# Kernel tuning notes

Hardware: AMD Instinct MI355X
Metric: run time of the kernel (lower is better)

Reference implementation:

```python
import jax, jax.numpy as jnp
import numpy as np
from jax import lax

B = 16384
N_NUM = 32
N_CAT = 16
D = 256
D_HID = 512
N_LAYERS = 8
VOCAB = 100001  # total_cats + 1
OUT_DIM = 2
TOT_FEAT = N_NUM + N_CAT
EPS = 1e-5


def _layernorm(x, g, b):
    mu = jnp.mean(x, axis=-1, keepdims=True)
    var = jnp.mean(jnp.square(x - mu), axis=-1, keepdims=True)
    return (x - mu) * lax.rsqrt(var + EPS) * g + b


def setup_inputs() -> dict:
    key = jax.random.key(0)
    ks = jax.random.split(key, 16)
    s = 0.02
    return {
        "x_numerical": jax.random.normal(ks[0], (B, N_NUM, 1), dtype=jnp.float32),
        "x_categorical_idx": jax.random.randint(ks[1], (B, N_CAT), 0, VOCAB - 1, dtype=jnp.int32),
        # per-feature Linear(1, D): weight [N_NUM, D], bias [N_NUM, D]
        "w_num": jax.random.normal(ks[2], (N_NUM, D), dtype=jnp.float32) * s,
        "b_num": jnp.zeros((N_NUM, D), dtype=jnp.float32),
        "cat_embed": jax.random.normal(ks[3], (VOCAB, D), dtype=jnp.float32) * s,
        "W_first": jax.random.normal(ks[4], (TOT_FEAT * D, D), dtype=jnp.float32) * s,
        "b_first": jnp.zeros((D,), dtype=jnp.float32),
        # stacked block params, leading dim = N_LAYERS
        "ln_g": jnp.ones((N_LAYERS, D), dtype=jnp.float32),
        "ln_b": jnp.zeros((N_LAYERS, D), dtype=jnp.float32),
        "W1s": jax.random.normal(ks[5], (N_LAYERS, D, D_HID), dtype=jnp.float32) * s,
        "b1s": jnp.zeros((N_LAYERS, D_HID), dtype=jnp.float32),
        "W2s": jax.random.normal(ks[6], (N_LAYERS, D_HID, D), dtype=jnp.float32) * s,
        "b2s": jnp.zeros((N_LAYERS, D), dtype=jnp.float32),
        "g_f": jnp.ones((D,), dtype=jnp.float32),
        "beta_f": jnp.zeros((D,), dtype=jnp.float32),
        "W_head": jax.random.normal(ks[7], (D, OUT_DIM), dtype=jnp.float32) * s,
        "b_head": jnp.zeros((OUT_DIM,), dtype=jnp.float32),
    }


def reference(x_numerical, x_categorical_idx, w_num, b_num, cat_embed,
              W_first, b_first, ln_g, ln_b, W1s, b1s, W2s, b2s,
              g_f, beta_f, W_head, b_head):
    # numerical embeddings: per-feature Linear(1, D), vectorized over features
    x_val = x_numerical[:, :, 0:1]                       # [B, N_NUM, 1]
    x_n_emb = x_val * w_num[None] + b_num[None]          # [B, N_NUM, D]
    x_c_emb = cat_embed[x_categorical_idx]               # [B, N_CAT, D]
    x = jnp.concatenate([x_n_emb, x_c_emb], axis=1)      # [B, TOT_FEAT, D]
    x = x.reshape(x.shape[0], -1)                        # [B, TOT_FEAT*D]
    x = x @ W_first + b_first                            # [B, D]

    def block(h, params):
        g, bn, W1, b1, W2, b2 = params
        out = _layernorm(h, g, bn)
        out = jax.nn.relu(out @ W1 + b1)                 # dropout = identity (eval)
        out = out @ W2 + b2
        return h + out, None

    x, _ = lax.scan(block, x, (ln_g, ln_b, W1s, b1s, W2s, b2s))
    x = _layernorm(x, g_f, beta_f)
    logits = x @ W_head + b_head                         # [B, OUT_DIM]
    return logits
```

## Files before the change

### kernel.cpp

```cpp
#include <hip/hip_runtime.h>

typedef unsigned short u16;
typedef unsigned int u32;
typedef __attribute__((ext_vector_type(8))) short bf16x8;
typedef __attribute__((ext_vector_type(4))) float f32x4;

#define LDK 72

__device__ __forceinline__ u16 f2bf(float f) {
    u32 u = __float_as_uint(f);
    u += 0x7fffu + ((u >> 16) & 1u);
    return (u16)(u >> 16);
}

__device__ __forceinline__ f32x4 mfma16(bf16x8 a, bf16x8 b, f32x4 c) {
    return __builtin_amdgcn_mfma_f32_16x16x32_bf16(a, b, c, 0, 0, 0);
}


__global__ __launch_bounds__(256) void prep_u_kernel(
    const float* __restrict__ w_num, const float* __restrict__ b_num,
    const float* __restrict__ W_first, float* __restrict__ U, float* __restrict__ P)
{
    __shared__ float wrow[256];
    __shared__ float brow[256];
    int j = threadIdx.x, f = blockIdx.x;
    wrow[j] = w_num[f * 256 + j];
    brow[j] = b_num[f * 256 + j];
    __syncthreads();
    float au = 0.f, ap = 0.f;
    for (int k = 0; k < 256; k++) {
        float w = W_first[(size_t)((f << 8) + k) * 256 + j];
        au = fmaf(wrow[k], w, au);
        ap = fmaf(brow[k], w, ap);
    }
    U[f * 256 + j] = au;
    P[f * 256 + j] = ap;
}

__global__ __launch_bounds__(256) void prep_c0_kernel(
    const float* __restrict__ b_first, const float* __restrict__ P, float* __restrict__ c0)
{
    int j = threadIdx.x;
    float a = b_first[j];
    for (int f = 0; f < 32; f++) a += P[f * 256 + j];
    c0[j] = a;
}

__global__ __launch_bounds__(256) void transpose_kernel(
    const float* __restrict__ in, u16* __restrict__ out,
    int R, int C, int ldo, int k_off, size_t in_stride, size_t out_stride)
{
    __shared__ float t[64][65];
    in  += (size_t)blockIdx.z * in_stride;
    out += (size_t)blockIdx.z * out_stride;
    const int tid = threadIdx.x;
    const int r0 = blockIdx.x * 64, c0 = blockIdx.y * 64;
#pragma unroll
    for (int i = 0; i < 16; i++) {
        int e = tid + i * 256;
        int r = e >> 6, c = e & 63;
        float v = (r0 + r < R) ? in[(size_t)(r0 + r) * C + c0 + c] : 0.f;
        t[c][r] = v;
    }
    __syncthreads();
#pragma unroll
    for (int i = 0; i < 2; i++) {
        int e = tid + i * 256;
        int c = e >> 3, r8 = (e & 7) * 8;
        u16 tmp[8];
#pragma unroll
        for (int x = 0; x < 8; x++) tmp[x] = f2bf(t[c][r8 + x]);
        *(bf16x8*)&out[(size_t)(c0 + c) * ldo + k_off + r0 + r8] = *(bf16x8*)tmp;
    }
}

#define FBM 32

#define GATHER(KQ, G0, G1)                                                    \
    {                                                                         \
        int chunk = tid;                                                      \
        int r = chunk >> 4, c4 = chunk & 15;                                  \
        int k = (KQ) + c4 * 4;                                                \
        if (k < 4096) {                                                       \
            int rowi = sidx[r * 16 + (k >> 8)];                               \
            G0 = *(const float4*)&cemb[(size_t)rowi * 256 + (k & 255)];       \
        } else if (k < 4128) {                                                \
            int c = k - 4096;                                                 \
            G0.x = sx[r * 32 + c];     G0.y = sx[r * 32 + c + 1];             \
            G0.z = sx[r * 32 + c + 2]; G0.w = sx[r * 32 + c + 3];             \
        } else G0 = make_float4(0.f, 0.f, 0.f, 0.f);                          \
        chunk = tid + 256;                                                    \
        r = chunk >> 4; c4 = chunk & 15;                                      \
        k = (KQ) + c4 * 4;                                                    \
        if (k < 4096) {                                                       \
            int rowi = sidx[r * 16 + (k >> 8)];                               \
            G1 = *(const float4*)&cemb[(size_t)rowi * 256 + (k & 255)];       \
        } else if (k < 4128) {                                                \
            int c = k - 4096;                                                 \
            G1.x = sx[r * 32 + c];     G1.y = sx[r * 32 + c + 1];             \
            G1.z = sx[r * 32 + c + 2]; G1.w = sx[r * 32 + c + 3];             \
        } else G1 = make_float4(0.f, 0.f, 0.f, 0.f);                          \
    }

__global__ __launch_bounds__(256) void first_gemm_kernel(
    const u16* __restrict__ BT, const float* __restrict__ bias,
    float* __restrict__ outF,
    const int* __restrict__ cidx, const float* __restrict__ cemb,
    const float* __restrict__ xnum)
{
    __shared__ __align__(16) u16 Ab[2][FBM * LDK];
    __shared__ __align__(16) u16 Bb[2][256 * 64];
    __shared__ int   sidx[FBM * 16];
    __shared__ float sx[FBM * 32];

    const int tid = threadIdx.x;
    const int lane = tid & 63;
    const int wv = tid >> 6;
    const int quad = lane >> 4;
    const int l16 = lane & 15;
    const int m0 = blockIdx.x * FBM;

#pragma unroll
    for (int i = 0; i < 2; i++) sidx[tid + i * 256] = cidx[m0 * 16 + tid + i * 256];
    {
        float4 v = *(const float4*)&xnum[(size_t)m0 * 32 + tid * 4];
        sx[tid * 4 + 0] = v.x; sx[tid * 4 + 1] = v.y;
        sx[tid * 4 + 2] = v.z; sx[tid * 4 + 3] = v.w;
    }
    __syncthreads();

    f32x4 acc[2][4];
#pragma unroll
    for (int i = 0; i < 2; i++)
#pragma unroll
        for (int j = 0; j < 4; j++) acc[i][j] = (f32x4){0.f, 0.f, 0.f, 0.f};

#define WRITE_A(BUF, G0, G1)                                                  \
    {                                                                         \
        int r = tid >> 4, c4 = tid & 15;                                      \
        u16* dst = &Ab[BUF][r * LDK + c4 * 4];                                \
        dst[0] = f2bf(G0.x); dst[1] = f2bf(G0.y);                             \
        dst[2] = f2bf(G0.z); dst[3] = f2bf(G0.w);                             \
        int chunk = tid + 256;                                                \
        r = chunk >> 4; c4 = chunk & 15;                                      \
        dst = &Ab[BUF][r * LDK + c4 * 4];                                     \
        dst[0] = f2bf(G1.x); dst[1] = f2bf(G1.y);                             \
        dst[2] = f2bf(G1.z); dst[3] = f2bf(G1.w);                             \
    }

#define DMA_B(BUF, KQ)                                                        \
    _Pragma("unroll")                                                         \
    for (int it = 0; it < 8; it++) {                                          \
        int chunk = it * 256 + tid;                                           \
        int r = chunk >> 3;                                                   \
        int c8 = (chunk & 7) ^ (r & 7);                                       \
        const u16* src = &BT[(size_t)r * 4160 + (KQ) + c8 * 8];               \
        __builtin_amdgcn_global_load_lds(                                     \
            (const __attribute__((address_space(1))) void*)src,               \
            (__attribute__((address_space(3))) void*)&Bb[BUF][(it * 256 + wv * 64) * 8], \
            16, 0, 0);                                                        \
    }

    float4 ga0, ga1;
    GATHER(0, ga0, ga1);
    WRITE_A(0, ga0, ga1);
    DMA_B(0, 0);
    GATHER(64, ga0, ga1);
    __syncthreads();

    for (int k0 = 0; k0 < 4160; k0 += 64) {
        const int cur = (k0 >> 6) & 1, nxt = cur ^ 1;
        if (k0 + 64 < 4160) {
            WRITE_A(nxt, ga0, ga1);
            DMA_B(nxt, k0 + 64);
            if (k0 + 128 < 4160) GATHER(k0 + 128, ga0, ga1);
        }
#pragma unroll
        for (int kk = 0; kk < 64; kk += 32) {
            bf16x8 af[2], bfr[4];
#pragma unroll
            for (int i = 0; i < 2; i++)
                af[i] = *(const bf16x8*)&Ab[cur][(i * 16 + l16) * LDK + kk + quad * 8];
#pragma unroll
            for (int j = 0; j < 4; j++) {
                int row = wv * 64 + j * 16 + l16;
                int c8L = quad + (kk >> 3);
                bfr[j] = *(const bf16x8*)&Bb[cur][row * 64 + ((c8L ^ (row & 7)) * 8)];
            }
#pragma unroll
            for (int i = 0; i < 2; i++)
#pragma unroll
                for (int j = 0; j < 4; j++)
                    acc[i][j] = mfma16(af[i], bfr[j], acc[i][j]);
        }
        __syncthreads();
    }

#pragma unroll
    for (int i = 0; i < 2; i++) {
#pragma unroll
        for (int j = 0; j < 4; j++) {
            int col = wv * 64 + j * 16 + l16;
            float bs = bias[col];
#pragma unroll
            for (int r = 0; r < 4; r++) {
                int row = m0 + i * 16 + quad * 4 + r;
                outF[(size_t)row * 256 + col] = acc[i][j][r] + bs;
            }
        }
    }
}

__global__ __launch_bounds__(512, 2) void layer_kernel(
    float* __restrict__ h,
    const float* __restrict__ g, const float* __restrict__ bta,
    const u16* __restrict__ W1, const float* __restrict__ b1,
    const u16* __restrict__ W2, const float* __restrict__ b2)
{
    __shared__ __align__(16) u16 hn[64 * 264];
    __shared__ __align__(16) u16 hid[64 * 520];
    const int tid  = threadIdx.x;
    const int lane = tid & 63;
    const int wv   = tid >> 6;
    const int quad = lane >> 4;
    const int l16  = lane & 15;
    const int m0   = blockIdx.x * 64;

    float4 gv4 = *(const float4*)&g[lane * 4];
    float4 bv4 = *(const float4*)&bta[lane * 4];
#pragma unroll
    for (int rr = 0; rr < 8; rr++) {
        int row = rr * 8 + wv;
        float4 x = *(const float4*)&h[(size_t)(m0 + row) * 256 + lane * 4];
        float s  = x.x + x.y + x.z + x.w;
        float s2 = x.x * x.x + x.y * x.y + x.z * x.z + x.w * x.w;
#pragma unroll
        for (int o = 32; o > 0; o >>= 1) { s += __shfl_xor(s, o); s2 += __shfl_xor(s2, o); }
        float mu = s * (1.f / 256.f);
        float rs = rsqrtf(s2 * (1.f / 256.f) - mu * mu + 1e-5f);
        ushort4 o4;
        o4.x = f2bf((x.x - mu) * rs * gv4.x + bv4.x);
        o4.y = f2bf((x.y - mu) * rs * gv4.y + bv4.y);
        o4.z = f2bf((x.z - mu) * rs * gv4.z + bv4.z);
        o4.w = f2bf((x.w - mu) * rs * gv4.w + bv4.w);
        *(ushort4*)&hn[row * 264 + lane * 4] = o4;
    }
    __syncthreads();

    float b1v[4];
#pragma unroll
    for (int j = 0; j < 4; j++) b1v[j] = b1[wv * 64 + j * 16 + l16];
    f32x4 acc1[4][4];
#pragma unroll
    for (int i = 0; i < 4; i++)
#pragma unroll
        for (int j = 0; j < 4; j++) acc1[i][j] = (f32x4){0.f, 0.f, 0.f, 0.f};
#pragma unroll
    for (int kk = 0; kk < 256; kk += 32) {
        bf16x8 af[4], bw[4];
#pragma unroll
        for (int i = 0; i < 4; i++)
            af[i] = *(const bf16x8*)&hn[(i * 16 + l16) * 264 + kk + quad * 8];
#pragma unroll
        for (int j = 0; j < 4; j++)
            bw[j] = *(const bf16x8*)&W1[(size_t)(wv * 64 + j * 16 + l16) * 256 + kk + quad * 8];
#pragma unroll
        for (int i = 0; i < 4; i++)
#pragma unroll
            for (int j = 0; j < 4; j++)
                acc1[i][j] = mfma16(af[i], bw[j], acc1[i][j]);
    }
#pragma unroll
    for (int i = 0; i < 4; i++)
#pragma unroll
        for (int j = 0; j < 4; j++)
#pragma unroll
            for (int r = 0; r < 4; r++) {
                float v = acc1[i][j][r] + b1v[j];
                v = v > 0.f ? v : 0.f;
                hid[(i * 16 + quad * 4 + r) * 520 + wv * 64 + j * 16 + l16] = f2bf(v);
            }
    __syncthreads();

    float b2v[2];
#pragma unroll
    for (int j = 0; j < 2; j++) b2v[j] = b2[wv * 32 + j * 16 + l16];
    f32x4 acc2[4][2];
#pragma unroll
    for (int i = 0; i < 4; i++)
#pragma unroll
        for (int j = 0; j < 2; j++) acc2[i][j] = (f32x4){0.f, 0.f, 0.f, 0.f};
#pragma unroll
    for (int kk = 0; kk < 512; kk += 32) {
        bf16x8 af[4], bw[2];
#pragma unroll
        for (int i = 0; i < 4; i++)
            af[i] = *(const bf16x8*)&hid[(i * 16 + l16) * 520 + kk + quad * 8];
#pragma unroll
        for (int j = 0; j < 2; j++)
            bw[j] = *(const bf16x8*)&W2[(size_t)(wv * 32 + j * 16 + l16) * 512 + kk + quad * 8];
#pragma unroll
        for (int i = 0; i < 4; i++)
#pragma unroll
            for (int j = 0; j < 2; j++)
                acc2[i][j] = mfma16(af[i], bw[j], acc2[i][j]);
    }
    __syncthreads();

    float* hstore = (float*)hid;
#pragma unroll
    for (int i = 0; i < 4; i++)
#pragma unroll
        for (int j = 0; j < 2; j++) {
            int col = wv * 32 + j * 16 + l16;
#pragma unroll
            for (int r = 0; r < 4; r++)
                hstore[(i * 16 + quad * 4 + r) * 260 + col] = acc2[i][j][r] + b2v[j];
        }
    __syncthreads();
#pragma unroll
    for (int rr = 0; rr < 8; rr++) {
        int row = rr * 8 + wv;
        float4 v = *(const float4*)&hstore[row * 260 + lane * 4];
        float4 res = *(const float4*)&h[(size_t)(m0 + row) * 256 + lane * 4];
        v.x += res.x; v.y += res.y; v.z += res.z; v.w += res.w;
        *(float4*)&h[(size_t)(m0 + row) * 256 + lane * 4] = v;
    }
}

__global__ __launch_bounds__(256) void head_kernel(
    const float* __restrict__ h, const float* __restrict__ g,
    const float* __restrict__ bta, const float* __restrict__ Wh,
    const float* __restrict__ bh, float* __restrict__ out)
{
    int lane = threadIdx.x & 63;
    int row = blockIdx.x * 4 + (threadIdx.x >> 6);
    const float4 x = *(const float4*)&h[(size_t)row * 256 + lane * 4];
    float s = x.x + x.y + x.z + x.w;
    float s2 = x.x * x.x + x.y * x.y + x.z * x.z + x.w * x.w;
    for (int o = 32; o > 0; o >>= 1) { s += __shfl_xor(s, o); s2 += __shfl_xor(s2, o); }
    float mu = s * (1.f / 256.f);
    float rs = rsqrtf(s2 * (1.f / 256.f) - mu * mu + 1e-5f);
    float4 gv = *(const float4*)&g[lane * 4];
    float4 bv = *(const float4*)&bta[lane * 4];
    float xn0 = (x.x - mu) * rs * gv.x + bv.x;
    float xn1 = (x.y - mu) * rs * gv.y + bv.y;
    float xn2 = (x.z - mu) * rs * gv.z + bv.z;
    float xn3 = (x.w - mu) * rs * gv.w + bv.w;
    float4 wa = *(const float4*)&Wh[lane * 8];
    float4 wb = *(const float4*)&Wh[lane * 8 + 4];
    float d0 = xn0 * wa.x + xn1 * wa.z + xn2 * wb.x + xn3 * wb.z;
    float d1 = xn0 * wa.y + xn1 * wa.w + xn2 * wb.y + xn3 * wb.w;
    for (int o = 32; o > 0; o >>= 1) { d0 += __shfl_xor(d0, o); d1 += __shfl_xor(d1, o); }
    if (lane == 0) {
        out[(size_t)row * 2 + 0] = d0 + bh[0];
        out[(size_t)row * 2 + 1] = d1 + bh[1];
    }
}

extern "C" void kernel_launch(void* const* d_in, const int* in_sizes, int n_in,
                              void* d_out, int out_size, void* d_ws, size_t ws_size,
                              hipStream_t stream)
{
    const float* x_num   = (const float*)d_in[0];
    const int*   cidx    = (const int*)d_in[1];
    const float* w_num   = (const float*)d_in[2];
    const float* b_num   = (const float*)d_in[3];
    const float* cemb    = (const float*)d_in[4];
    const float* W_first = (const float*)d_in[5];
    const float* b_first = (const float*)d_in[6];
    const float* ln_g    = (const float*)d_in[7];
    const float* ln_b    = (const float*)d_in[8];
    const float* W1s     = (const float*)d_in[9];
    const float* b1s     = (const float*)d_in[10];
    const float* W2s     = (const float*)d_in[11];
    const float* b2s     = (const float*)d_in[12];
    const float* g_f     = (const float*)d_in[13];
    const float* beta_f  = (const float*)d_in[14];
    const float* W_head  = (const float*)d_in[15];
    const float* b_head  = (const float*)d_in[16];
    float* out = (float*)d_out;

    char* ws = (char*)d_ws;
    float* U   = (float*)(ws + 0);
    float* c0  = (float*)(ws + 32768);
    float* P   = (float*)(ws + 33792);
    u16* WcT   = (u16*)(ws + 66560);
    u16* W1T   = (u16*)(ws + 2196480);
    u16* W2T   = (u16*)(ws + 4293632);
    float* h   = (float*)(ws + 6390784);

    prep_u_kernel<<<32, 256, 0, stream>>>(w_num, b_num, W_first, U, P);
    prep_c0_kernel<<<1, 256, 0, stream>>>(b_first, P, c0);
    transpose_kernel<<<dim3(64, 4, 1), 256, 0, stream>>>(
        W_first + (size_t)8192 * 256, WcT, 4096, 256, 4160, 0, 0, 0);
    transpose_kernel<<<dim3(1, 4, 1), 256, 0, stream>>>(
        U, WcT, 32, 256, 4160, 4096, 0, 0);
    transpose_kernel<<<dim3(4, 8, 8), 256, 0, stream>>>(
        W1s, W1T, 256, 512, 256, 0, 131072, 131072);
    transpose_kernel<<<dim3(8, 4, 8), 256, 0, stream>>>(
        W2s, W2T, 512, 256, 512, 0, 131072, 131072);

    first_gemm_kernel<<<512, 256, 0, stream>>>(
        WcT, c0, h, cidx, cemb, x_num);

    for (int l = 0; l < 8; l++) {
        layer_kernel<<<256, 512, 0, stream>>>(
            h, ln_g + l * 256, ln_b + l * 256,
            W1T + (size_t)l * 131072, b1s + l * 512,
            W2T + (size_t)l * 131072, b2s + l * 256);
    }
    head_kernel<<<4096, 256, 0, stream>>>(h, g_f, beta_f, W_head, b_head, out);
}
```

Measured before the change: 507.3 us.

## Double row tile in first GEMM and deepen gather prefetch with manual waitcnt pipelining

The first GEMM now uses 64-row tiles with 512 threads and 8 waves arranged 2x4, which halves the number of times each weight tile is streamed per batch row. The main loop is unrolled by two with two register sets of gathered embeddings, so gathers are issued two stages ahead. Explicit s_waitcnt and sched_barrier calls replace __syncthreads. Gathers are made branch-free with vector LDS stores. The cost is higher register pressure and fragile hand-written wait counts, which could cause correctness hazards if the vmcnt values are wrong.

New measurement: 497.6 us. No clear change (-1.9%).

```diff
diff --git a/kernel.cpp b/kernel.cpp
--- a/kernel.cpp
+++ b/kernel.cpp
@@ -29,6 +29,7 @@
     brow[j] = b_num[f * 256 + j];
     __syncthreads();
     float au = 0.f, ap = 0.f;
+#pragma unroll 8
     for (int k = 0; k < 256; k++) {
         float w = W_first[(size_t)((f << 8) + k) * 256 + j];
         au = fmaf(wrow[k], w, au);
@@ -43,6 +44,7 @@
 {
     int j = threadIdx.x;
     float a = b_first[j];
+#pragma unroll 8
     for (int f = 0; f < 32; f++) a += P[f * 256 + j];
     c0[j] = a;
 }
@@ -75,137 +77,156 @@
     }
 }
 
-#define FBM 32
+#define FBM 64
 
 #define GATHER(KQ, G0, G1)                                                    \
     {                                                                         \
         int chunk = tid;                                                      \
         int r = chunk >> 4, c4 = chunk & 15;                                  \
         int k = (KQ) + c4 * 4;                                                \
-        if (k < 4096) {                                                       \
-            int rowi = sidx[r * 16 + (k >> 8)];                               \
-            G0 = *(const float4*)&cemb[(size_t)rowi * 256 + (k & 255)];       \
-        } else if (k < 4128) {                                                \
-            int c = k - 4096;                                                 \
-            G0.x = sx[r * 32 + c];     G0.y = sx[r * 32 + c + 1];             \
-            G0.z = sx[r * 32 + c + 2]; G0.w = sx[r * 32 + c + 3];             \
-        } else G0 = make_float4(0.f, 0.f, 0.f, 0.f);                          \
-        chunk = tid + 256;                                                    \
+        int rowi = (k < 4096) ? sidx[r * 16 + ((k >> 8) & 15)] : 0;           \
+        G0 = *(const float4*)&cemb[(size_t)rowi * 256 + (k & 255)];           \
+        if (k >= 4096) {                                                      \
+            if (k < 4128) {                                                   \
+                int c = r * 32 + (k - 4096);                                  \
+                G0.x = sx[c]; G0.y = sx[c + 1];                               \
+                G0.z = sx[c + 2]; G0.w = sx[c + 3];                           \
+            } else G0 = make_float4(0.f, 0.f, 0.f, 0.f);                      \
+        }                                                                     \
+        chunk = tid + 512;                                                    \
         r = chunk >> 4; c4 = chunk & 15;                                      \
         k = (KQ) + c4 * 4;                                                    \
-        if (k < 4096) {                                                       \
-            int rowi = sidx[r * 16 + (k >> 8)];                               \
-            G1 = *(const float4*)&cemb[(size_t)rowi * 256 + (k & 255)];       \
-        } else if (k < 4128) {                                                \
-            int c = k - 4096;                                                 \
-            G1.x = sx[r * 32 + c];     G1.y = sx[r * 32 + c + 1];             \
-            G1.z = sx[r * 32 + c + 2]; G1.w = sx[r * 32 + c + 3];             \
-        } else G1 = make_float4(0.f, 0.f, 0.f, 0.f);                          \
-    }
-
-__global__ __launch_bounds__(256) void first_gemm_kernel(
-    const u16* __restrict__ BT, const float* __restrict__ bias,
-    float* __restrict__ outF,
-    const int* __restrict__ cidx, const float* __restrict__ cemb,
-    const float* __restrict__ xnum)
-{
-    __shared__ __align__(16) u16 Ab[2][FBM * LDK];
-    __shared__ __align__(16) u16 Bb[2][256 * 64];
-    __shared__ int   sidx[FBM * 16];
-    __shared__ float sx[FBM * 32];
-
-    const int tid = threadIdx.x;
-    const int lane = tid & 63;
-    const int wv = tid >> 6;
-    const int quad = lane >> 4;
-    const int l16 = lane & 15;
-    const int m0 = blockIdx.x * FBM;
-
-#pragma unroll
-    for (int i = 0; i < 2; i++) sidx[tid + i * 256] = cidx[m0 * 16 + tid + i * 256];
-    {
-        float4 v = *(const float4*)&xnum[(size_t)m0 * 32 + tid * 4];
-        sx[tid * 4 + 0] = v.x; sx[tid * 4 + 1] = v.y;
-        sx[tid * 4 + 2] = v.z; sx[tid * 4 + 3] = v.w;
-    }
-    __syncthreads();
-
-    f32x4 acc[2][4];
-#pragma unroll
-    for (int i = 0; i < 2; i++)
-#pragma unroll
-        for (int j = 0; j < 4; j++) acc[i][j] = (f32x4){0.f, 0.f, 0.f, 0.f};
+        rowi = (k < 4096) ? sidx[r * 16 + ((k >> 8) & 15)] : 0;               \
+        G1 = *(const float4*)&cemb[(size_t)rowi * 256 + (k & 255)];           \
+        if (k >= 4096) {                                                      \
+            if (k < 4128) {                                                   \
+                int c = r * 32 + (k - 4096);                                  \
+                G1.x = sx[c]; G1.y = sx[c + 1];                               \
+                G1.z = sx[c + 2]; G1.w = sx[c + 3];                           \
+            } else G1 = make_float4(0.f, 0.f, 0.f, 0.f);                      \
+        }                                                                     \
+    }
 
 #define WRITE_A(BUF, G0, G1)                                                  \
     {                                                                         \
-        int r = tid >> 4, c4 = tid & 15;                                      \
-        u16* dst = &Ab[BUF][r * LDK + c4 * 4];                                \
-        dst[0] = f2bf(G0.x); dst[1] = f2bf(G0.y);                             \
-        dst[2] = f2bf(G0.z); dst[3] = f2bf(G0.w);                             \
-        int chunk = tid + 256;                                                \
+        int chunk = tid;                                                      \
+        int r = chunk >> 4, c4 = chunk & 15;                                  \
+        ushort4 o;                                                            \
+        o.x = f2bf(G0.x); o.y = f2bf(G0.y); o.z = f2bf(G0.z); o.w = f2bf(G0.w); \
+        *(ushort4*)&Ab[BUF][r * LDK + c4 * 4] = o;                            \
+        chunk = tid + 512;                                                    \
         r = chunk >> 4; c4 = chunk & 15;                                      \
-        dst = &Ab[BUF][r * LDK + c4 * 4];                                     \
-        dst[0] = f2bf(G1.x); dst[1] = f2bf(G1.y);                             \
-        dst[2] = f2bf(G1.z); dst[3] = f2bf(G1.w);                             \
+        o.x = f2bf(G1.x); o.y = f2bf(G1.y); o.z = f2bf(G1.z); o.w = f2bf(G1.w); \
+        *(ushort4*)&Ab[BUF][r * LDK + c4 * 4] = o;                            \
     }
 
 #define DMA_B(BUF, KQ)                                                        \
     _Pragma("unroll")                                                         \
-    for (int it = 0; it < 8; it++) {                                          \
-        int chunk = it * 256 + tid;                                           \
+    for (int it = 0; it < 4; it++) {                                          \
+        int chunk = it * 512 + tid;                                           \
         int r = chunk >> 3;                                                   \
         int c8 = (chunk & 7) ^ (r & 7);                                       \
         const u16* src = &BT[(size_t)r * 4160 + (KQ) + c8 * 8];               \
         __builtin_amdgcn_global_load_lds(                                     \
             (const __attribute__((address_space(1))) void*)src,               \
-            (__attribute__((address_space(3))) void*)&Bb[BUF][(it * 256 + wv * 64) * 8], \
+            (__attribute__((address_space(3))) void*)&Bb[BUF][(it * 512 + wv * 64) * 8], \
             16, 0, 0);                                                        \
     }
 
-    float4 ga0, ga1;
-    GATHER(0, ga0, ga1);
-    WRITE_A(0, ga0, ga1);
+#define COMPUTE(CUR)                                                          \
+    _Pragma("unroll")                                                         \
+    for (int kk = 0; kk < 64; kk += 32) {                                     \
+        bf16x8 af[2], bfr[4];                                                 \
+        _Pragma("unroll")                                                     \
+        for (int i = 0; i < 2; i++)                                           \
+            af[i] = *(const bf16x8*)&Ab[CUR][(wm * 32 + i * 16 + l16) * LDK + kk + quad * 8]; \
+        _Pragma("unroll")                                                     \
+        for (int j = 0; j < 4; j++) {                                         \
+            int row = wn * 64 + j * 16 + l16;                                 \
+            int c8L = quad + (kk >> 3);                                       \
+            bfr[j] = *(const bf16x8*)&Bb[CUR][row * 64 + ((c8L ^ (row & 7)) * 8)]; \
+        }                                                                     \
+        _Pragma("unroll")                                                     \
+        for (int i = 0; i < 2; i++)                                           \
+            _Pragma("unroll")                                                 \
+            for (int j = 0; j < 4; j++)                                       \
+                acc[i][j] = mfma16(af[i], bfr[j], acc[i][j]);                 \
+    }
+
+#define ITER_MAIN(CUR, KQ, GA0, GA1)                                          \
+    {                                                                         \
+        WRITE_A(CUR ^ 1, GA0, GA1);                                           \
+        DMA_B(CUR ^ 1, (KQ) + 64);                                            \
+        __builtin_amdgcn_sched_barrier(0);                                    \
+        GATHER((KQ) + 192, GA0, GA1);                                         \
+        COMPUTE(CUR);                                                         \
+        asm volatile("s_waitcnt vmcnt(2) lgkmcnt(0)" ::: "memory");           \
+        __builtin_amdgcn_s_barrier();                                         \
+        __builtin_amdgcn_sched_barrier(0);                                    \
+    }
+
+__global__ __launch_bounds__(512, 2) void first_gemm_kernel(
+    const u16* __restrict__ BT, const float* __restrict__ bias,
+    float* __restrict__ outF,
+    const int* __restrict__ cidx, const float* __restrict__ cemb,
+    const float* __restrict__ xnum)
+{
+    __shared__ __align__(16) u16 Ab[2][FBM * LDK];
+    __shared__ __align__(16) u16 Bb[2][256 * 64];
+    __shared__ int   sidx[FBM * 16];
+    __shared__ float sx[FBM * 32];
+
+    const int tid  = threadIdx.x;
+    const int lane = tid & 63;
+    const int wv   = tid >> 6;
+    const int wm   = wv >> 2;
+    const int wn   = wv & 3;
+    const int quad = lane >> 4;
+    const int l16  = lane & 15;
+    const int m0   = blockIdx.x * FBM;
+
+    sidx[tid]       = cidx[m0 * 16 + tid];
+    sidx[tid + 512] = cidx[m0 * 16 + tid + 512];
+    {
+        float4 v = *(const float4*)&xnum[(size_t)m0 * 32 + tid * 4];
+        *(float4*)&sx[tid * 4] = v;
+    }
+    __syncthreads();
+
+    f32x4 acc[2][4];
+#pragma unroll
+    for (int i = 0; i < 2; i++)
+#pragma unroll
+        for (int j = 0; j < 4; j++) acc[i][j] = (f32x4){0.f, 0.f, 0.f, 0.f};
+
+    float4 pa0, pa1, pb0, pb1;
+
+    GATHER(0, pa0, pa1);
+    WRITE_A(0, pa0, pa1);
     DMA_B(0, 0);
-    GATHER(64, ga0, ga1);
-    __syncthreads();
-
-    for (int k0 = 0; k0 < 4160; k0 += 64) {
-        const int cur = (k0 >> 6) & 1, nxt = cur ^ 1;
-        if (k0 + 64 < 4160) {
-            WRITE_A(nxt, ga0, ga1);
-            DMA_B(nxt, k0 + 64);
-            if (k0 + 128 < 4160) GATHER(k0 + 128, ga0, ga1);
-        }
-#pragma unroll
-        for (int kk = 0; kk < 64; kk += 32) {
-            bf16x8 af[2], bfr[4];
-#pragma unroll
-            for (int i = 0; i < 2; i++)
-                af[i] = *(const bf16x8*)&Ab[cur][(i * 16 + l16) * LDK + kk + quad * 8];
-#pragma unroll
-            for (int j = 0; j < 4; j++) {
-                int row = wv * 64 + j * 16 + l16;
-                int c8L = quad + (kk >> 3);
-                bfr[j] = *(const bf16x8*)&Bb[cur][row * 64 + ((c8L ^ (row & 7)) * 8)];
-            }
-#pragma unroll
-            for (int i = 0; i < 2; i++)
-#pragma unroll
-                for (int j = 0; j < 4; j++)
-                    acc[i][j] = mfma16(af[i], bfr[j], acc[i][j]);
-        }
-        __syncthreads();
-    }
+    __builtin_amdgcn_sched_barrier(0);
+    GATHER(64, pa0, pa1);
+    GATHER(128, pb0, pb1);
+    asm volatile("s_waitcnt vmcnt(4) lgkmcnt(0)" ::: "memory");
+    __builtin_amdgcn_s_barrier();
+    __builtin_amdgcn_sched_barrier(0);
+
+#pragma unroll 1
+    for (int k0 = 0; k0 < 4096; k0 += 128) {
+        ITER_MAIN(0, k0,      pa0, pa1);
+        ITER_MAIN(1, k0 + 64, pb0, pb1);
+    }
+    COMPUTE(0);
 
 #pragma unroll
     for (int i = 0; i < 2; i++) {
 #pragma unroll
         for (int j = 0; j < 4; j++) {
-            int col = wv * 64 + j * 16 + l16;
+            int col = wn * 64 + j * 16 + l16;
             float bs = bias[col];
 #pragma unroll
             for (int r = 0; r < 4; r++) {
-                int row = m0 + i * 16 + quad * 4 + r;
+                int row = m0 + wm * 32 + i * 16 + quad * 4 + r;
                 outF[(size_t)row * 256 + col] = acc[i][j][r] + bs;
             }
         }
@@ -402,7 +423,7 @@
     transpose_kernel<<<dim3(8, 4, 8), 256, 0, stream>>>(
         W2s, W2T, 512, 256, 512, 0, 131072, 131072);
 
-    first_gemm_kernel<<<512, 256, 0, stream>>>(
+    first_gemm_kernel<<<256, 512, 0, stream>>>(
         WcT, c0, h, cidx, cemb, x_num);
 
     for (int l = 0; l < 8; l++) {
```
